# Kernel tuning notes

Hardware: AMD Instinct MI355X
Metric: run time of the kernel (lower is better)

## Reference

```python
import jax, jax.numpy as jnp
import numpy as np

D, H, DFF = 256, 8, 2048
Q, E, WORD = 36, 8, 20
S = 32768 + WORD * E  # 32928 total memory tokens


def _ln(x, g, b, eps=1e-5):
    m = x.mean(-1, keepdims=True)
    v = ((x - m) ** 2).mean(-1, keepdims=True)
    return (x - m) / jnp.sqrt(v + eps) * g + b


def _mha(q, k, v, w_in, b_in, w_out, b_out, nhead, key_pad=None):
    # q: [E,Lq,d], k/v: [E,Lk,d], key_pad: [E,Lk] bool (True = masked)
    e, lq, d = q.shape
    lk = k.shape[1]
    dh = d // nhead
    wq, wk, wv = w_in[:d], w_in[d:2 * d], w_in[2 * d:]
    bq, bk, bv = b_in[:d], b_in[d:2 * d], b_in[2 * d:]
    qp = (q @ wq.T + bq).reshape(e, lq, nhead, dh)
    kp = (k @ wk.T + bk).reshape(e, lk, nhead, dh)
    vp = (v @ wv.T + bv).reshape(e, lk, nhead, dh)
    s = jnp.einsum('eqhd,ekhd->ehqk', qp, kp) / jnp.sqrt(jnp.asarray(dh, qp.dtype))
    if key_pad is not None:
        s = jnp.where(key_pad[:, None, None, :], jnp.asarray(-1e9, s.dtype), s)
    a = jax.nn.softmax(s, axis=-1)
    o = jnp.einsum('ehqk,ekhd->eqhd', a, vp).reshape(e, lq, d)
    return o @ w_out.T + b_out


def setup_inputs() -> dict:
    key = jax.random.key(0)
    ks = jax.random.split(key, 16)
    sc = 0.02
    return {
        'tgt': jax.random.normal(ks[0], (Q, 1, D), jnp.float32),
        'memory': jax.random.normal(ks[1], (S, 1, D), jnp.float32),
        'memory_key_padding_mask': jnp.zeros((1, S), jnp.bool_),
        'pos': jax.random.normal(ks[2], (S, 1, D), jnp.float32),
        'query_pos': jax.random.normal(ks[3], (Q, 1, D), jnp.float32),
        'no_of_exps': E,
        'sa_w_in': sc * jax.random.normal(ks[4], (3 * D, D), jnp.float32),
        'sa_b_in': jnp.zeros((3 * D,), jnp.float32),
        'sa_w_out': sc * jax.random.normal(ks[5], (D, D), jnp.float32),
        'sa_b_out': jnp.zeros((D,), jnp.float32),
        'ca_w_in': sc * jax.random.normal(ks[6], (3 * D, D), jnp.float32),
        'ca_b_in': jnp.zeros((3 * D,), jnp.float32),
        'ca_w_out': sc * jax.random.normal(ks[7], (D, D), jnp.float32),
        'ca_b_out': jnp.zeros((D,), jnp.float32),
        'w1': sc * jax.random.normal(ks[8], (DFF, D), jnp.float32),
        'b1': jnp.zeros((DFF,), jnp.float32),
        'w2': sc * jax.random.normal(ks[9], (D, DFF), jnp.float32),
        'b2': jnp.zeros((D,), jnp.float32),
        'ln1_g': jnp.ones((D,), jnp.float32), 'ln1_b': jnp.zeros((D,), jnp.float32),
        'ln2_g': jnp.ones((D,), jnp.float32), 'ln2_b': jnp.zeros((D,), jnp.float32),
        'ln3_g': jnp.ones((D,), jnp.float32), 'ln3_b': jnp.zeros((D,), jnp.float32),
    }


def reference(tgt, memory, memory_key_padding_mask, pos, query_pos, no_of_exps,
              sa_w_in, sa_b_in, sa_w_out, sa_b_out,
              ca_w_in, ca_b_in, ca_w_out, ca_b_out,
              w1, b1, w2, b2,
              ln1_g, ln1_b, ln2_g, ln2_b, ln3_g, ln3_b):
    e = int(no_of_exps)
    q_len, _, d = tgt.shape
    s_tot = memory.shape[0]
    s_sub = s_tot - WORD * e
    # repeat tgt / query_pos to experts, move expert to batch dim: [E,Q,d]
    x = jnp.broadcast_to(tgt, (q_len, e, d)).transpose(1, 0, 2)
    qp = jnp.broadcast_to(query_pos, (q_len, e, d)).transpose(1, 0, 2)
    # --- self attention (per expert, q=k=tgt+query_pos, v=tgt) ---
    qk = x + qp
    sa = _mha(qk, qk, x, sa_w_in, sa_b_in, sa_w_out, sa_b_out, H)
    x = _ln(x + sa, ln1_g, ln1_b)
    # --- per-expert memory: shared sub_memory + expert word window ---
    mem = memory[:, 0]          # [S,d]
    pmem = pos[:, 0]            # [S,d]
    kpm = memory_key_padding_mask[0]  # [S]
    sub = jnp.broadcast_to(mem[:s_sub], (e, s_sub, d))
    win = mem[s_sub:].reshape(e, WORD, d)
    kv = jnp.concatenate([sub, win], axis=1)            # [E, s_sub+WORD, d]
    psub = jnp.broadcast_to(pmem[:s_sub], (e, s_sub, d))
    pwin = pmem[s_sub:].reshape(e, WORD, d)
    pkv = jnp.concatenate([psub, pwin], axis=1)
    kpm_e = jnp.concatenate([jnp.broadcast_to(kpm[:s_sub], (e, s_sub)),
                             kpm[s_sub:].reshape(e, WORD)], axis=1)
    # --- cross attention ---
    ca = _mha(x + qp, kv + pkv, kv, ca_w_in, ca_b_in, ca_w_out, ca_b_out, H, kpm_e)
    x = _ln(x + ca, ln2_g, ln2_b)
    # --- FFN ---
    ff = jax.nn.relu(x @ w1.T + b1) @ w2.T + b2
    x = _ln(x + ff, ln3_g, ln3_b)
    # torch code cats per-expert [Q,1,d] along dim=1 -> [Q,E,d]
    return x.transpose(1, 0, 2)
```

## Files before the change

### kernel.cpp

```cpp
#include <hip/hip_runtime.h>
#include <math.h>

#define D_ 256
#define H_ 8
#define Q_ 36
#define E_ 8
#define WORD_ 20
#define S_ 32928
#define SSUB_ 32768
#define DFF_ 2048
#define NCHUNK 256
#define KC 128

typedef unsigned int u32;
typedef unsigned short u16;
typedef unsigned long long u64;
typedef float f4 __attribute__((ext_vector_type(4)));
typedef short bf8 __attribute__((ext_vector_type(8)));
typedef short s4v __attribute__((ext_vector_type(4)));

__device__ __forceinline__ u16 f2bf(float f) {
    u32 u = __float_as_uint(f);
    u32 r = u + 0x7fffu + ((u >> 16) & 1u);
    return (u16)(r >> 16);
}
__device__ __forceinline__ float bf2f(u16 h) { return __uint_as_float(((u32)h) << 16); }

__device__ __forceinline__ f4 mfma16(bf8 a, bf8 b, f4 c) {
    return __builtin_amdgcn_mfma_f32_16x16x32_bf16(a, b, c, 0, 0, 0);
}

__device__ __forceinline__ void block_ln_stats(float v, float* red, float* red2, int tid,
                                               float& mean, float& var) {
    red[tid] = v; red2[tid] = v * v;
    __syncthreads();
    for (int st = 128; st > 0; st >>= 1) {
        if (tid < st) { red[tid] += red[tid + st]; red2[tid] += red2[tid + st]; }
        __syncthreads();
    }
    mean = red[0] * (1.f / 256.f);
    var = red2[0] * (1.f / 256.f) - mean * mean;
    __syncthreads();
}

__global__ void __launch_bounds__(256) k_wcvt(const float* __restrict__ caw,
                                              const float* __restrict__ w1,
                                              const float* __restrict__ w2,
                                              u16* __restrict__ wkvbf,
                                              u16* __restrict__ w1bf,
                                              u16* __restrict__ w2bf) {
    int i = (blockIdx.x * 256 + threadIdx.x) * 4;
    const float* src; u16* dst; int off;
    if (i < 131072) { src = caw + 65536; dst = wkvbf; off = i; }
    else if (i < 655360) { src = w1; dst = w1bf; off = i - 131072; }
    else { src = w2; dst = w2bf; off = i - 655360; }
    float4 v = *(const float4*)(src + off);
    ushort4 o;
    o.x = f2bf(v.x); o.y = f2bf(v.y); o.z = f2bf(v.z); o.w = f2bf(v.w);
    *(ushort4*)(dst + off) = o;
}

__global__ void __launch_bounds__(512, 2) k_kv(const float* __restrict__ mem,
                                               const float* __restrict__ pos,
                                               const u16* __restrict__ wkvbf,
                                               const float* __restrict__ cab,
                                               u16* __restrict__ Kca, u16* __restrict__ Vca) {
    __shared__ u16 smem[4][64 * 64];
    char* const base = (char*)smem;
    const int tid = threadIdx.x;
    const int lane = tid & 63, wid = tid >> 6;
    const int lr = lane & 15, lg = lane >> 4;
    const int s0 = blockIdx.x * 64;
    const int kv = wid >> 2;
    const int cb = (wid & 3) * 64;
    const u16* wb = wkvbf + kv * 65536;

    const int srow = tid >> 3;
    const int scol = (tid & 7) * 8;
    int sg = s0 + srow; if (sg >= S_) sg = S_ - 1;
    const float* mp = mem + (u64)sg * 256 + scol;
    const float* pp = pos + (u64)sg * 256 + scol;
    const int sboff = (srow * 128 + scol * 2) ^ ((srow & 7) << 4);

    f4 acc[4][4];
#pragma unroll
    for (int i = 0; i < 4; i++)
#pragma unroll
        for (int j = 0; j < 4; j++) acc[i][j] = (f4){0.f, 0.f, 0.f, 0.f};

    float4 Lm0[2], Lm1[2], Lp0[2], Lp1[2];
    Lm0[0] = *(const float4*)(mp);
    Lm1[0] = *(const float4*)(mp + 4);
    Lp0[0] = *(const float4*)(pp);
    Lp1[0] = *(const float4*)(pp + 4);

#pragma unroll
    for (int ks = 0; ks < 4; ks++) {
        const int cur = ks & 1, nxt = cur ^ 1;
        if (ks < 3) {
            Lm0[nxt] = *(const float4*)(mp + (ks + 1) * 64);
            Lm1[nxt] = *(const float4*)(mp + (ks + 1) * 64 + 4);
            Lp0[nxt] = *(const float4*)(pp + (ks + 1) * 64);
            Lp1[nxt] = *(const float4*)(pp + (ks + 1) * 64 + 4);
        }
        u16 tk[8], tv[8];
        tk[0] = f2bf(Lm0[cur].x + Lp0[cur].x); tk[1] = f2bf(Lm0[cur].y + Lp0[cur].y);
        tk[2] = f2bf(Lm0[cur].z + Lp0[cur].z); tk[3] = f2bf(Lm0[cur].w + Lp0[cur].w);
        tk[4] = f2bf(Lm1[cur].x + Lp1[cur].x); tk[5] = f2bf(Lm1[cur].y + Lp1[cur].y);
        tk[6] = f2bf(Lm1[cur].z + Lp1[cur].z); tk[7] = f2bf(Lm1[cur].w + Lp1[cur].w);
        tv[0] = f2bf(Lm0[cur].x); tv[1] = f2bf(Lm0[cur].y);
        tv[2] = f2bf(Lm0[cur].z); tv[3] = f2bf(Lm0[cur].w);
        tv[4] = f2bf(Lm1[cur].x); tv[5] = f2bf(Lm1[cur].y);
        tv[6] = f2bf(Lm1[cur].z); tv[7] = f2bf(Lm1[cur].w);
        char* AbK = base + cur * 16384;
        char* AbV = AbK + 8192;
        *(bf8*)(AbK + sboff) = *(bf8*)tk;
        *(bf8*)(AbV + sboff) = *(bf8*)tv;
        __syncthreads();
        char* Ab = kv ? AbV : AbK;
#pragma unroll
        for (int kk = 0; kk < 2; kk++) {
            bf8 af[4], bfr[4];
#pragma unroll
            for (int b = 0; b < 4; b++) {
                int row = b * 16 + lr;
                af[b] = *(const bf8*)(Ab + ((row * 128 + kk * 64 + lg * 16) ^ ((row & 7) << 4)));
            }
#pragma unroll
            for (int a = 0; a < 4; a++) {
                int n = cb + a * 16 + lr;
                bfr[a] = *(const bf8*)(wb + (u64)n * 256 + ks * 64 + kk * 32 + lg * 8);
            }
            if (kv == 0) {
#pragma unroll
                for (int a = 0; a < 4; a++)
#pragma unroll
                    for (int b = 0; b < 4; b++)
                        acc[a][b] = mfma16(bfr[a], af[b], acc[a][b]);
            } else {
#pragma unroll
                for (int a = 0; a < 4; a++)
#pragma unroll
                    for (int b = 0; b < 4; b++)
                        acc[a][b] = mfma16(af[a], bfr[b], acc[a][b]);
            }
        }
        __syncthreads();
    }

    if (kv == 0) {
        float biasK[4][4];
#pragma unroll
        for (int a = 0; a < 4; a++)
#pragma unroll
            for (int r = 0; r < 4; r++) biasK[a][r] = cab[256 + cb + a * 16 + lg * 4 + r];
#pragma unroll
        for (int a = 0; a < 4; a++)
#pragma unroll
            for (int b = 0; b < 4; b++) {
                int nn = cb + a * 16 + lg * 4;
                int s = b * 16 + lr;
                u16 t4[4];
#pragma unroll
                for (int r = 0; r < 4; r++) t4[r] = f2bf(acc[a][b][r] + biasK[a][r]);
                *(s4v*)(base + ((s * 512 + nn * 2) ^ ((s & 7) << 4))) = *(s4v*)t4;
            }
    }
    __syncthreads();
#pragma unroll
    for (int i = 0; i < 4; i++) {
        int c = tid + i * 512;
        int s = c >> 5, oct = c & 31;
        if (s0 + s < S_) {
            bf8 v = *(const bf8*)(base + ((s * 512 + oct * 16) ^ ((s & 7) << 4)));
            int h = oct >> 2, nl = (oct & 3) * 8;
            *(bf8*)(Kca + ((u64)h * S_ + s0 + s) * 32 + nl) = v;
        }
    }
    __syncthreads();
    if (kv == 1) {
#pragma unroll
        for (int b = 0; b < 4; b++) {
            int n = cb + b * 16 + lr;
            float bias = cab[512 + n];
#pragma unroll
            for (int a = 0; a < 4; a++) {
                int sb = a * 16 + lg * 4;
                u16 t4[4];
#pragma unroll
                for (int r = 0; r < 4; r++) t4[r] = f2bf(acc[a][b][r] + bias);
                *(s4v*)(base + ((n * 128 + sb * 2) ^ ((n & 7) << 4))) = *(s4v*)t4;
            }
        }
    }
    __syncthreads();
#pragma unroll
    for (int i = 0; i < 4; i++) {
        int c = tid + i * 512;
        int n = c >> 3, oct = c & 7;
        int ss = s0 + oct * 8;
        if (ss < S_) {
            bf8 v = *(const bf8*)(base + ((n * 128 + oct * 16) ^ ((n & 7) << 4)));
            *(bf8*)(Vca + (u64)n * S_ + ss) = v;
        }
    }
}

__global__ void __launch_bounds__(256) k_saproj(const float* __restrict__ tgt,
                                                const float* __restrict__ qpos,
                                                const float* __restrict__ w,
                                                const float* __restrict__ bvec,
                                                float* __restrict__ qkv) {
    int bx = blockIdx.x;
    int mat = bx / 36, row = bx % 36;
    int n = threadIdx.x;
    __shared__ float xr[256];
    float tv = tgt[row * 256 + n];
    xr[n] = (mat < 2) ? tv + qpos[row * 256 + n] : tv;
    __syncthreads();
    const float* wr_ = w + (u64)(mat * 256 + n) * 256;
    float acc = bvec[mat * 256 + n];
    for (int k = 0; k < 256; k++) acc += xr[k] * wr_[k];
    qkv[(u64)bx * 256 + n] = acc;
}

__global__ void __launch_bounds__(256) k_saattn(const float* __restrict__ qkv,
                                                float* __restrict__ osa) {
    int hh = blockIdx.x;
    int tid = threadIdx.x;
    __shared__ float qh[36][32], kh[36][32], vh[36][32];
    __shared__ float sc[36][40];
    for (int i = tid; i < 36 * 32; i += 256) {
        int rr = i >> 5, dd = i & 31;
        qh[rr][dd] = qkv[(u64)(0 + rr) * 256 + hh * 32 + dd];
        kh[rr][dd] = qkv[(u64)(36 + rr) * 256 + hh * 32 + dd];
        vh[rr][dd] = qkv[(u64)(72 + rr) * 256 + hh * 32 + dd];
    }
    __syncthreads();
    for (int i = tid; i < 36 * 36; i += 256) {
        int qi = i / 36, ki = i % 36;
        float s = 0.f;
        for (int k2 = 0; k2 < 32; k2++) s += qh[qi][k2] * kh[ki][k2];
        sc[qi][ki] = s * 0.17677669529663687f;
    }
    __syncthreads();
    if (tid < 36) {
        float mx = sc[tid][0];
        for (int k = 1; k < 36; k++) mx = fmaxf(mx, sc[tid][k]);
        float zz = 0.f;
        for (int k = 0; k < 36; k++) { float p = __expf(sc[tid][k] - mx); sc[tid][k] = p; zz += p; }
        float inv = 1.f / zz;
        for (int k = 0; k < 36; k++) sc[tid][k] *= inv;
    }
    __syncthreads();
    for (int i = tid; i < 36 * 32; i += 256) {
        int qi = i >> 5, dd = i & 31;
        float s = 0.f;
        for (int k2 = 0; k2 < 36; k2++) s += sc[qi][k2] * vh[k2][dd];
        osa[(u64)qi * 256 + hh * 32 + dd] = s;
    }
}

__global__ void __launch_bounds__(256) k_ln1(const float* __restrict__ osa,
                                             const float* __restrict__ tgt,
                                             const float* __restrict__ qpos,
                                             const float* __restrict__ swout,
                                             const float* __restrict__ sbout,
                                             const float* __restrict__ g1,
                                             const float* __restrict__ b1ln,
                                             const float* __restrict__ caw,
                                             const float* __restrict__ cab,
                                             float* __restrict__ x1, float* __restrict__ qca) {
    int q = blockIdx.x;
    int n = threadIdx.x;
    __shared__ float orow[256], xq[256], red[256], red2[256];
    orow[n] = osa[(u64)q * 256 + n];
    __syncthreads();
    float acc = sbout[n] + tgt[q * 256 + n];
    const float* wr_ = swout + (u64)n * 256;
    for (int k = 0; k < 256; k++) acc += orow[k] * wr_[k];
    float mean, var;
    block_ln_stats(acc, red, red2, n, mean, var);
    float rstd = rsqrtf(var + 1e-5f);
    float val = (acc - mean) * rstd * g1[n] + b1ln[n];
    x1[(u64)q * 256 + n] = val;
    xq[n] = val + qpos[q * 256 + n];
    __syncthreads();
    float a2 = cab[n];
    const float* wr2 = caw + (u64)n * 256;
    for (int k = 0; k < 256; k++) a2 += xq[k] * wr2[k];
    qca[(u64)q * 256 + n] = a2 * 0.17677669529663687f;
}

__global__ void __launch_bounds__(256) k_flash(const float* __restrict__ qca,
                                               const u16* __restrict__ Kca,
                                               const u16* __restrict__ Vca,
                                               u16* __restrict__ nump,
                                               float* __restrict__ mzp) {
    __shared__ u16 pT[4][48 * 64];
    const int tid = threadIdx.x;
    const int lane = tid & 63, wslot = tid >> 6;
    const int gw = blockIdx.x * 4 + wslot;
    const int h = gw >> 8, chunk = gw & 255;
    const int lr = lane & 15, lg = lane >> 4;
    char* pb = (char*)pT[wslot];

    bf8 qf[3];
#pragma unroll
    for (int nt = 0; nt < 3; nt++) {
        int q = nt * 16 + lr;
        u16 t8[8];
        if (q < Q_) {
            const float* p = qca + (u64)q * 256 + h * 32 + lg * 8;
#pragma unroll
            for (int j = 0; j < 8; j++) t8[j] = f2bf(p[j]);
        } else {
#pragma unroll
            for (int j = 0; j < 8; j++) t8[j] = 0;
        }
        qf[nt] = *(bf8*)t8;
    }
    f4 numT[2][3];
#pragma unroll
    for (int mi = 0; mi < 2; mi++)
#pragma unroll
        for (int nt = 0; nt < 3; nt++) numT[mi][nt] = (f4){0.f, 0.f, 0.f, 0.f};
    float mrun[3] = {-3e38f, -3e38f, -3e38f};
    float zl[3] = {0.f, 0.f, 0.f};
    const int base = chunk * KC;
    const f4 z4 = (f4){0.f, 0.f, 0.f, 0.f};

    for (int b = 0; b < 2; b++) {
        int kb0 = base + b * 64;
        f4 st[4][3];
#pragma unroll
        for (int kt = 0; kt < 4; kt++) {
            bf8 af = *(const bf8*)(Kca + ((u64)h * S_ + kb0 + kt * 16 + lr) * 32 + lg * 8);
#pragma unroll
            for (int nt = 0; nt < 3; nt++) st[kt][nt] = mfma16(af, qf[nt], z4);
        }
#pragma unroll
        for (int nt = 0; nt < 3; nt++) {
            float mx = -3e38f;
#pragma unroll
            for (int kt = 0; kt < 4; kt++)
#pragma unroll
                for (int r = 0; r < 4; r++) mx = fmaxf(mx, st[kt][nt][r]);
            mx = fmaxf(mx, __shfl_xor(mx, 16));
            mx = fmaxf(mx, __shfl_xor(mx, 32));
            float mnew = fmaxf(mrun[nt], mx);
            float al = __expf(mrun[nt] - mnew);
            mrun[nt] = mnew;
            float zs = 0.f;
#pragma unroll
            for (int kt = 0; kt < 4; kt++)
#pragma unroll
                for (int r = 0; r < 4; r++) {
                    float p = __expf(st[kt][nt][r] - mnew);
                    st[kt][nt][r] = p;
                    zs += p;
                }
            zl[nt] = zl[nt] * al + zs;
#pragma unroll
            for (int mi = 0; mi < 2; mi++)
#pragma unroll
                for (int r = 0; r < 4; r++) numT[mi][nt][r] *= al;
            int qrow = nt * 16 + lr;
            int swz = (qrow & 7) << 4;
#pragma unroll
            for (int kt = 0; kt < 4; kt++)
#pragma unroll
                for (int r = 0; r < 4; r += 2) {
                    int keyl = kt * 16 + lg * 4 + r;
                    u32 pk = (u32)f2bf(st[kt][nt][r]) | ((u32)f2bf(st[kt][nt][r + 1]) << 16);
                    *(u32*)(pb + qrow * 128 + ((keyl * 2) ^ swz)) = pk;
                }
        }
#pragma unroll
        for (int kb = 0; kb < 2; kb++) {
            bf8 pf[3];
#pragma unroll
            for (int nt = 0; nt < 3; nt++) {
                int qrow = nt * 16 + lr;
                pf[nt] = *(const bf8*)(pb + qrow * 128 + ((kb * 64 + lg * 16) ^ ((qrow & 7) << 4)));
            }
#pragma unroll
            for (int mi = 0; mi < 2; mi++) {
                bf8 vf = *(const bf8*)(Vca + ((u64)(h * 32 + mi * 16 + lr)) * S_ + kb0 + kb * 32 + lg * 8);
#pragma unroll
                for (int nt = 0; nt < 3; nt++) numT[mi][nt] = mfma16(vf, pf[nt], numT[mi][nt]);
            }
        }
    }
#pragma unroll
    for (int nt = 0; nt < 3; nt++) {
        float z = zl[nt];
        z += __shfl_xor(z, 16);
        z += __shfl_xor(z, 32);
        int q = nt * 16 + lr;
        if (lg == 0 && q < Q_) {
            u64 o = ((u64)(h * 36 + q) * NCHUNK + chunk) * 2;
            mzp[o] = mrun[nt];
            mzp[o + 1] = z;
        }
    }
#pragma unroll
    for (int mi = 0; mi < 2; mi++)
#pragma unroll
        for (int nt = 0; nt < 3; nt++) {
            int q = nt * 16 + lr;
            if (q < Q_) {
#pragma unroll
                for (int r = 0; r < 4; r++)
                    nump[((u64)(h * 36 + q) * NCHUNK + chunk) * 32 + mi * 16 + lg * 4 + r] =
                        f2bf(numT[mi][nt][r]);
            }
        }
}

__global__ void __launch_bounds__(64) k_merge(const float* __restrict__ mzp,
                                              const u16* __restrict__ nump,
                                              float* __restrict__ ssum) {
    int idx = blockIdx.x;
    int lane = threadIdx.x;
    float m[4], z[4];
#pragma unroll
    for (int j = 0; j < 4; j++) {
        m[j] = mzp[((u64)idx * NCHUNK + j * 64 + lane) * 2];
        z[j] = mzp[((u64)idx * NCHUNK + j * 64 + lane) * 2 + 1];
    }
    float M = fmaxf(fmaxf(m[0], m[1]), fmaxf(m[2], m[3]));
    for (int o = 1; o < 64; o <<= 1) M = fmaxf(M, __shfl_xor(M, o));
    float w[4], Z = 0.f;
#pragma unroll
    for (int j = 0; j < 4; j++) { w[j] = __expf(m[j] - M); Z += z[j] * w[j]; }
    for (int o = 1; o < 64; o <<= 1) Z += __shfl_xor(Z, o);
    __shared__ float buf[64][33];
#pragma unroll
    for (int d = 0; d < 32; d++) {
        float s = 0.f;
#pragma unroll
        for (int j = 0; j < 4; j++)
            s += bf2f(nump[((u64)idx * NCHUNK + j * 64 + lane) * 32 + d]) * w[j];
        buf[lane][d] = s;
    }
    __syncthreads();
    if (lane < 32) {
        float s = 0.f;
        for (int c = 0; c < 64; c++) s += buf[c][lane];
        ssum[(u64)idx * 34 + 2 + lane] = s;
    }
    if (lane == 0) { ssum[(u64)idx * 34] = M; ssum[(u64)idx * 34 + 1] = Z; }
}

__global__ void __launch_bounds__(256) k_combine(const float* __restrict__ qca,
                                                 const u16* __restrict__ Kca,
                                                 const u16* __restrict__ Vca,
                                                 const float* __restrict__ ssum,
                                                 const float* __restrict__ x1,
                                                 const float* __restrict__ wout,
                                                 const float* __restrict__ bout,
                                                 const float* __restrict__ g2,
                                                 const float* __restrict__ b2ln,
                                                 float* __restrict__ x2f, u16* __restrict__ x2h) {
    int bx = blockIdx.x;
    int e = bx / 36, q = bx % 36;
    int tid = threadIdx.x;
    __shared__ float pw[8][20], Mh[8], Zh[8], Ssc[8], o[256], red[256], red2[256];
    int h = tid >> 5, d = tid & 31;
    if (d < WORD_) {
        int key = SSUB_ + e * WORD_ + d;
        const float* qp = qca + (u64)q * 256 + h * 32;
        const u16* kp = Kca + ((u64)h * S_ + key) * 32;
        float s = 0.f;
        for (int k = 0; k < 32; k++) s += qp[k] * bf2f(kp[k]);
        pw[h][d] = s;
    }
    __syncthreads();
    if (tid < 8) {
        int hh = tid, ih = hh * 36 + q;
        float Ms = ssum[(u64)ih * 34], Zs = ssum[(u64)ih * 34 + 1];
        float mw = pw[hh][0];
        for (int w = 1; w < WORD_; w++) mw = fmaxf(mw, pw[hh][w]);
        float Me = fmaxf(Ms, mw);
        float Zw = 0.f;
        for (int w = 0; w < WORD_; w++) { float p = __expf(pw[hh][w] - Me); pw[hh][w] = p; Zw += p; }
        float sc = __expf(Ms - Me);
        Mh[hh] = Me; Zh[hh] = Zs * sc + Zw; Ssc[hh] = sc;
    }
    __syncthreads();
    {
        int ih = h * 36 + q;
        float num = ssum[(u64)ih * 34 + 2 + d] * Ssc[h];
        const u16* vp = Vca + ((u64)(h * 32 + d)) * S_ + SSUB_ + e * WORD_;
        for (int w = 0; w < WORD_; w++) num += pw[h][w] * bf2f(vp[w]);
        o[tid] = num / Zh[h];
    }
    __syncthreads();
    int n = tid;
    float acc = bout[n] + x1[(u64)q * 256 + n];
    const float* wr_ = wout + (u64)n * 256;
    for (int k = 0; k < 256; k++) acc += o[k] * wr_[k];
    float mean, var;
    block_ln_stats(acc, red, red2, n, mean, var);
    float rstd = rsqrtf(var + 1e-5f);
    float val = (acc - mean) * rstd * g2[n] + b2ln[n];
    x2f[(u64)bx * 256 + n] = val;
    x2h[(u64)bx * 256 + n] = f2bf(val);
}

__global__ void __launch_bounds__(64) k_ffn1(const u16* __restrict__ x2h,
                                             const u16* __restrict__ w1bf,
                                             const float* __restrict__ b1,
                                             u16* __restrict__ hbuf) {
    const int lane = threadIdx.x & 63;
    const int lr = lane & 15, lg = lane >> 4;
    const int s0 = blockIdx.x * 16, n0 = blockIdx.y * 64;

    f4 acc[4];
#pragma unroll
    for (int ni = 0; ni < 4; ni++) acc[ni] = (f4){0.f, 0.f, 0.f, 0.f};

#pragma unroll
    for (int k0 = 0; k0 < 8; k0++) {
        bf8 a = *(const bf8*)(x2h + (u64)(s0 + lr) * 256 + k0 * 32 + lg * 8);
#pragma unroll
        for (int ni = 0; ni < 4; ni++) {
            bf8 b = *(const bf8*)(w1bf + (u64)(n0 + ni * 16 + lr) * 256 + k0 * 32 + lg * 8);
            acc[ni] = mfma16(b, a, acc[ni]);
        }
    }
#pragma unroll
    for (int ni = 0; ni < 4; ni++) {
        int n = n0 + ni * 16 + lg * 4;
        float4 bi = *(const float4*)(b1 + n);
        u16 t4[4];
        t4[0] = f2bf(fmaxf(acc[ni][0] + bi.x, 0.f));
        t4[1] = f2bf(fmaxf(acc[ni][1] + bi.y, 0.f));
        t4[2] = f2bf(fmaxf(acc[ni][2] + bi.z, 0.f));
        t4[3] = f2bf(fmaxf(acc[ni][3] + bi.w, 0.f));
        *(s4v*)(hbuf + (u64)(s0 + lr) * 2048 + n) = *(s4v*)t4;
    }
}

__global__ void __launch_bounds__(256) k_ffn2(const u16* __restrict__ hbuf,
                                              const u16* __restrict__ w2bf,
                                              float* __restrict__ ypart) {
    const int tid = threadIdx.x;
    const int lane = tid & 63, wid = tid >> 6;
    const int lr = lane & 15, lg = lane >> 4;
    const int s0 = blockIdx.x * 16, kc = blockIdx.y;

    f4 acc[4];
#pragma unroll
    for (int ni = 0; ni < 4; ni++) acc[ni] = (f4){0.f, 0.f, 0.f, 0.f};

#pragma unroll
    for (int k0 = 0; k0 < 8; k0++) {
        bf8 a = *(const bf8*)(hbuf + (u64)(s0 + lr) * 2048 + kc * 256 + k0 * 32 + lg * 8);
#pragma unroll
        for (int ni = 0; ni < 4; ni++) {
            bf8 b = *(const bf8*)(w2bf + (u64)(wid * 64 + ni * 16 + lr) * 2048 + kc * 256 + k0 * 32 + lg * 8);
            acc[ni] = mfma16(b, a, acc[ni]);
        }
    }
#pragma unroll
    for (int ni = 0; ni < 4; ni++) {
        int n = wid * 64 + ni * 16 + lg * 4;
        *(f4*)(ypart + ((u64)kc * 288 + s0 + lr) * 256 + n) = acc[ni];
    }
}

__global__ void __launch_bounds__(256) k_ln3(const float* __restrict__ ypart,
                                             const float* __restrict__ b2,
                                             const float* __restrict__ x2f,
                                             const float* __restrict__ g3,
                                             const float* __restrict__ b3,
                                             float* __restrict__ out) {
    int r = blockIdx.x;
    int e = r / 36, q = r - e * 36;
    int n = threadIdx.x;
    __shared__ float red[256], red2[256];
    float v = x2f[(u64)r * 256 + n] + b2[n];
#pragma unroll
    for (int kc = 0; kc < 8; kc++) v += ypart[((u64)kc * 288 + r) * 256 + n];
    float mean, var;
    block_ln_stats(v, red, red2, n, mean, var);
    float rstd = rsqrtf(var + 1e-5f);
    float val = (v - mean) * rstd * g3[n] + b3[n];
    out[((u64)q * E_ + e) * 256 + n] = val;
}

extern "C" void kernel_launch(void* const* d_in, const int* in_sizes, int n_in,
                              void* d_out, int out_size, void* d_ws, size_t ws_size,
                              hipStream_t stream) {
    const float* tgt = (const float*)d_in[0];
    const float* mem = (const float*)d_in[1];
    const float* pos = (const float*)d_in[3];
    const float* qpos = (const float*)d_in[4];
    const float* sa_w_in = (const float*)d_in[6];
    const float* sa_b_in = (const float*)d_in[7];
    const float* sa_w_out = (const float*)d_in[8];
    const float* sa_b_out = (const float*)d_in[9];
    const float* ca_w_in = (const float*)d_in[10];
    const float* ca_b_in = (const float*)d_in[11];
    const float* ca_w_out = (const float*)d_in[12];
    const float* ca_b_out = (const float*)d_in[13];
    const float* w1 = (const float*)d_in[14];
    const float* b1 = (const float*)d_in[15];
    const float* w2 = (const float*)d_in[16];
    const float* b2 = (const float*)d_in[17];
    const float* g1 = (const float*)d_in[18];
    const float* bb1 = (const float*)d_in[19];
    const float* g2 = (const float*)d_in[20];
    const float* bb2 = (const float*)d_in[21];
    const float* g3 = (const float*)d_in[22];
    const float* bb3 = (const float*)d_in[23];
    float* out = (float*)d_out;

    char* ws = (char*)d_ws;
    u16* Kca    = (u16*)(ws);
    u16* Vca    = (u16*)(ws + 16859136);
    u16* wkvbf  = (u16*)(ws + 33718272);
    u16* w1bf   = (u16*)(ws + 33980416);
    u16* w2bf   = (u16*)(ws + 35028992);
    float* qkv  = (float*)(ws + 36077568);
    float* osa  = (float*)(ws + 36188160);
    float* x1   = (float*)(ws + 36225024);
    float* qca  = (float*)(ws + 36261888);
    u16* nump   = (u16*)(ws + 36298752);
    u16* hbuf   = (u16*)(ws + 36298752);
    float* ypart= (float*)(ws + 37478400);
    float* mzp  = (float*)(ws + 41017344);
    float* ssum = (float*)(ws + 41607168);
    float* x2f  = (float*)(ws + 41646336);
    u16* x2h    = (u16*)(ws + 41941248);

    hipLaunchKernelGGL(k_wcvt, dim3(1152), dim3(256), 0, stream, ca_w_in, w1, w2, wkvbf, w1bf, w2bf);
    hipLaunchKernelGGL(k_kv, dim3(515), dim3(512), 0, stream, mem, pos, wkvbf, ca_b_in, Kca, Vca);
    hipLaunchKernelGGL(k_saproj, dim3(108), dim3(256), 0, stream, tgt, qpos, sa_w_in, sa_b_in, qkv);
    hipLaunchKernelGGL(k_saattn, dim3(8), dim3(256), 0, stream, qkv, osa);
    hipLaunchKernelGGL(k_ln1, dim3(36), dim3(256), 0, stream, osa, tgt, qpos, sa_w_out, sa_b_out,
                       g1, bb1, ca_w_in, ca_b_in, x1, qca);
    hipLaunchKernelGGL(k_flash, dim3(512), dim3(256), 0, stream, qca, Kca, Vca, nump, mzp);
    hipLaunchKernelGGL(k_merge, dim3(288), dim3(64), 0, stream, mzp, nump, ssum);
    hipLaunchKernelGGL(k_combine, dim3(288), dim3(256), 0, stream, qca, Kca, Vca, ssum, x1,
                       ca_w_out, ca_b_out, g2, bb2, x2f, x2h);
    hipLaunchKernelGGL(k_ffn1, dim3(18, 32), dim3(64), 0, stream, x2h, w1bf, b1, hbuf);
    hipLaunchKernelGGL(k_ffn2, dim3(18, 8), dim3(256), 0, stream, hbuf, w2bf, ypart);
    hipLaunchKernelGGL(k_ln3, dim3(288), dim3(256), 0, stream, ypart, b2, x2f, g3, bb3, out);
}
```

Baseline: 139.8 us.

## Preload full K tile in k_kv and use transposed bf16 small-GEMV weights

```diff
diff --git a/kernel.cpp b/kernel.cpp
--- a/kernel.cpp
+++ b/kernel.cpp
@@ -44,29 +44,59 @@
 }
 
 __global__ void __launch_bounds__(256) k_wcvt(const float* __restrict__ caw,
+                                              const float* __restrict__ saw,
+                                              const float* __restrict__ sow,
+                                              const float* __restrict__ cow,
                                               const float* __restrict__ w1,
                                               const float* __restrict__ w2,
                                               u16* __restrict__ wkvbf,
                                               u16* __restrict__ w1bf,
-                                              u16* __restrict__ w2bf) {
-    int i = (blockIdx.x * 256 + threadIdx.x) * 4;
-    const float* src; u16* dst; int off;
-    if (i < 131072) { src = caw + 65536; dst = wkvbf; off = i; }
-    else if (i < 655360) { src = w1; dst = w1bf; off = i - 131072; }
-    else { src = w2; dst = w2bf; off = i - 655360; }
-    float4 v = *(const float4*)(src + off);
-    ushort4 o;
-    o.x = f2bf(v.x); o.y = f2bf(v.y); o.z = f2bf(v.z); o.w = f2bf(v.w);
-    *(ushort4*)(dst + off) = o;
-}
-
-__global__ void __launch_bounds__(512, 2) k_kv(const float* __restrict__ mem,
+                                              u16* __restrict__ w2bf,
+                                              u16* __restrict__ saT,
+                                              u16* __restrict__ soT,
+                                              u16* __restrict__ caqT,
+                                              u16* __restrict__ coT) {
+    long i = ((long)blockIdx.x * 256 + threadIdx.x) * 4;
+    if (i < 1179648) {
+        const float* src; u16* dst; long off;
+        if (i < 131072) { src = caw + 65536; dst = wkvbf; off = i; }
+        else if (i < 655360) { src = w1; dst = w1bf; off = i - 131072; }
+        else { src = w2; dst = w2bf; off = i - 655360; }
+        float4 v = *(const float4*)(src + off);
+        ushort4 o;
+        o.x = f2bf(v.x); o.y = f2bf(v.y); o.z = f2bf(v.z); o.w = f2bf(v.w);
+        *(ushort4*)(dst + off) = o;
+    } else {
+        long j = i - 1179648;
+#pragma unroll
+        for (int t = 0; t < 4; t++) {
+            long e = j + t;
+            if (e < 196608) {
+                int n = e >> 8, k = e & 255;
+                saT[k * 768 + n] = f2bf(saw[e]);
+            } else if (e < 262144) {
+                long e2 = e - 196608; int n = e2 >> 8, k = e2 & 255;
+                soT[k * 256 + n] = f2bf(sow[e2]);
+            } else if (e < 327680) {
+                long e2 = e - 262144; int n = e2 >> 8, k = e2 & 255;
+                caqT[k * 256 + n] = f2bf(caw[e2]);
+            } else if (e < 393216) {
+                long e2 = e - 327680; int n = e2 >> 8, k = e2 & 255;
+                coT[k * 256 + n] = f2bf(cow[e2]);
+            }
+        }
+    }
+}
+
+__global__ void __launch_bounds__(512, 4) k_kv(const float* __restrict__ mem,
                                                const float* __restrict__ pos,
                                                const u16* __restrict__ wkvbf,
                                                const float* __restrict__ cab,
                                                u16* __restrict__ Kca, u16* __restrict__ Vca) {
-    __shared__ u16 smem[4][64 * 64];
-    char* const base = (char*)smem;
+    __shared__ u16 AK[64 * 256];
+    __shared__ u16 AV[64 * 256];
+    char* const bK = (char*)AK;
+    char* const bV = (char*)AV;
     const int tid = threadIdx.x;
     const int lane = tid & 63, wid = tid >> 6;
     const int lr = lane & 15, lg = lane >> 4;
@@ -76,11 +106,35 @@
     const u16* wb = wkvbf + kv * 65536;
 
     const int srow = tid >> 3;
-    const int scol = (tid & 7) * 8;
+    const int scol8 = (tid & 7) * 8;
     int sg = s0 + srow; if (sg >= S_) sg = S_ - 1;
-    const float* mp = mem + (u64)sg * 256 + scol;
-    const float* pp = pos + (u64)sg * 256 + scol;
-    const int sboff = (srow * 128 + scol * 2) ^ ((srow & 7) << 4);
+    const float* mp = mem + (u64)sg * 256 + scol8;
+    const float* pp = pos + (u64)sg * 256 + scol8;
+
+    float4 M0[4], M1[4], P0[4], P1[4];
+#pragma unroll
+    for (int g = 0; g < 4; g++) {
+        M0[g] = *(const float4*)(mp + g * 64);
+        M1[g] = *(const float4*)(mp + g * 64 + 4);
+        P0[g] = *(const float4*)(pp + g * 64);
+        P1[g] = *(const float4*)(pp + g * 64 + 4);
+    }
+#pragma unroll
+    for (int g = 0; g < 4; g++) {
+        u16 tk[8], tv[8];
+        tk[0] = f2bf(M0[g].x + P0[g].x); tk[1] = f2bf(M0[g].y + P0[g].y);
+        tk[2] = f2bf(M0[g].z + P0[g].z); tk[3] = f2bf(M0[g].w + P0[g].w);
+        tk[4] = f2bf(M1[g].x + P1[g].x); tk[5] = f2bf(M1[g].y + P1[g].y);
+        tk[6] = f2bf(M1[g].z + P1[g].z); tk[7] = f2bf(M1[g].w + P1[g].w);
+        tv[0] = f2bf(M0[g].x); tv[1] = f2bf(M0[g].y);
+        tv[2] = f2bf(M0[g].z); tv[3] = f2bf(M0[g].w);
+        tv[4] = f2bf(M1[g].x); tv[5] = f2bf(M1[g].y);
+        tv[6] = f2bf(M1[g].z); tv[7] = f2bf(M1[g].w);
+        int boff = (srow * 512 + (scol8 + g * 64) * 2) ^ ((srow & 7) << 4);
+        *(bf8*)(bK + boff) = *(bf8*)tk;
+        *(bf8*)(bV + boff) = *(bf8*)tv;
+    }
+    __syncthreads();
 
     f4 acc[4][4];
 #pragma unroll
@@ -88,65 +142,35 @@
 #pragma unroll
         for (int j = 0; j < 4; j++) acc[i][j] = (f4){0.f, 0.f, 0.f, 0.f};
 
-    float4 Lm0[2], Lm1[2], Lp0[2], Lp1[2];
-    Lm0[0] = *(const float4*)(mp);
-    Lm1[0] = *(const float4*)(mp + 4);
-    Lp0[0] = *(const float4*)(pp);
-    Lp1[0] = *(const float4*)(pp + 4);
-
-#pragma unroll
-    for (int ks = 0; ks < 4; ks++) {
-        const int cur = ks & 1, nxt = cur ^ 1;
-        if (ks < 3) {
-            Lm0[nxt] = *(const float4*)(mp + (ks + 1) * 64);
-            Lm1[nxt] = *(const float4*)(mp + (ks + 1) * 64 + 4);
-            Lp0[nxt] = *(const float4*)(pp + (ks + 1) * 64);
-            Lp1[nxt] = *(const float4*)(pp + (ks + 1) * 64 + 4);
-        }
-        u16 tk[8], tv[8];
-        tk[0] = f2bf(Lm0[cur].x + Lp0[cur].x); tk[1] = f2bf(Lm0[cur].y + Lp0[cur].y);
-        tk[2] = f2bf(Lm0[cur].z + Lp0[cur].z); tk[3] = f2bf(Lm0[cur].w + Lp0[cur].w);
-        tk[4] = f2bf(Lm1[cur].x + Lp1[cur].x); tk[5] = f2bf(Lm1[cur].y + Lp1[cur].y);
-        tk[6] = f2bf(Lm1[cur].z + Lp1[cur].z); tk[7] = f2bf(Lm1[cur].w + Lp1[cur].w);
-        tv[0] = f2bf(Lm0[cur].x); tv[1] = f2bf(Lm0[cur].y);
-        tv[2] = f2bf(Lm0[cur].z); tv[3] = f2bf(Lm0[cur].w);
-        tv[4] = f2bf(Lm1[cur].x); tv[5] = f2bf(Lm1[cur].y);
-        tv[6] = f2bf(Lm1[cur].z); tv[7] = f2bf(Lm1[cur].w);
-        char* AbK = base + cur * 16384;
-        char* AbV = AbK + 8192;
-        *(bf8*)(AbK + sboff) = *(bf8*)tk;
-        *(bf8*)(AbV + sboff) = *(bf8*)tv;
-        __syncthreads();
-        char* Ab = kv ? AbV : AbK;
-#pragma unroll
-        for (int kk = 0; kk < 2; kk++) {
-            bf8 af[4], bfr[4];
-#pragma unroll
-            for (int b = 0; b < 4; b++) {
-                int row = b * 16 + lr;
-                af[b] = *(const bf8*)(Ab + ((row * 128 + kk * 64 + lg * 16) ^ ((row & 7) << 4)));
-            }
-#pragma unroll
-            for (int a = 0; a < 4; a++) {
-                int n = cb + a * 16 + lr;
-                bfr[a] = *(const bf8*)(wb + (u64)n * 256 + ks * 64 + kk * 32 + lg * 8);
-            }
-            if (kv == 0) {
-#pragma unroll
-                for (int a = 0; a < 4; a++)
-#pragma unroll
-                    for (int b = 0; b < 4; b++)
-                        acc[a][b] = mfma16(bfr[a], af[b], acc[a][b]);
-            } else {
-#pragma unroll
-                for (int a = 0; a < 4; a++)
-#pragma unroll
-                    for (int b = 0; b < 4; b++)
-                        acc[a][b] = mfma16(af[a], bfr[b], acc[a][b]);
-            }
-        }
-        __syncthreads();
-    }
+    char* Ab = kv ? bV : bK;
+#pragma unroll
+    for (int kk = 0; kk < 8; kk++) {
+        bf8 af[4], bfr[4];
+#pragma unroll
+        for (int b = 0; b < 4; b++) {
+            int row = b * 16 + lr;
+            af[b] = *(const bf8*)(Ab + ((row * 512 + kk * 64 + lg * 16) ^ ((row & 7) << 4)));
+        }
+#pragma unroll
+        for (int a = 0; a < 4; a++) {
+            int n = cb + a * 16 + lr;
+            bfr[a] = *(const bf8*)(wb + (u64)n * 256 + kk * 32 + lg * 8);
+        }
+        if (kv == 0) {
+#pragma unroll
+            for (int a = 0; a < 4; a++)
+#pragma unroll
+                for (int b = 0; b < 4; b++)
+                    acc[a][b] = mfma16(bfr[a], af[b], acc[a][b]);
+        } else {
+#pragma unroll
+            for (int a = 0; a < 4; a++)
+#pragma unroll
+                for (int b = 0; b < 4; b++)
+                    acc[a][b] = mfma16(af[a], bfr[b], acc[a][b]);
+        }
+    }
+    __syncthreads();
 
     if (kv == 0) {
         float biasK[4][4];
@@ -163,8 +187,22 @@
                 u16 t4[4];
 #pragma unroll
                 for (int r = 0; r < 4; r++) t4[r] = f2bf(acc[a][b][r] + biasK[a][r]);
-                *(s4v*)(base + ((s * 512 + nn * 2) ^ ((s & 7) << 4))) = *(s4v*)t4;
+                *(s4v*)(bK + ((s * 512 + nn * 2) ^ ((s & 7) << 4))) = *(s4v*)t4;
             }
+    } else {
+#pragma unroll
+        for (int b = 0; b < 4; b++) {
+            int n = cb + b * 16 + lr;
+            float bias = cab[512 + n];
+#pragma unroll
+            for (int a = 0; a < 4; a++) {
+                int sb = a * 16 + lg * 4;
+                u16 t4[4];
+#pragma unroll
+                for (int r = 0; r < 4; r++) t4[r] = f2bf(acc[a][b][r] + bias);
+                *(s4v*)(bV + ((n * 128 + sb * 2) ^ ((n & 7) << 4))) = *(s4v*)t4;
+            }
+        }
     }
     __syncthreads();
 #pragma unroll
@@ -172,35 +210,18 @@
         int c = tid + i * 512;
         int s = c >> 5, oct = c & 31;
         if (s0 + s < S_) {
-            bf8 v = *(const bf8*)(base + ((s * 512 + oct * 16) ^ ((s & 7) << 4)));
+            bf8 v = *(const bf8*)(bK + ((s * 512 + oct * 16) ^ ((s & 7) << 4)));
             int h = oct >> 2, nl = (oct & 3) * 8;
             *(bf8*)(Kca + ((u64)h * S_ + s0 + s) * 32 + nl) = v;
         }
     }
-    __syncthreads();
-    if (kv == 1) {
-#pragma unroll
-        for (int b = 0; b < 4; b++) {
-            int n = cb + b * 16 + lr;
-            float bias = cab[512 + n];
-#pragma unroll
-            for (int a = 0; a < 4; a++) {
-                int sb = a * 16 + lg * 4;
-                u16 t4[4];
-#pragma unroll
-                for (int r = 0; r < 4; r++) t4[r] = f2bf(acc[a][b][r] + bias);
-                *(s4v*)(base + ((n * 128 + sb * 2) ^ ((n & 7) << 4))) = *(s4v*)t4;
-            }
-        }
-    }
-    __syncthreads();
 #pragma unroll
     for (int i = 0; i < 4; i++) {
         int c = tid + i * 512;
         int n = c >> 3, oct = c & 7;
         int ss = s0 + oct * 8;
         if (ss < S_) {
-            bf8 v = *(const bf8*)(base + ((n * 128 + oct * 16) ^ ((n & 7) << 4)));
+            bf8 v = *(const bf8*)(bV + ((n * 128 + oct * 16) ^ ((n & 7) << 4)));
             *(bf8*)(Vca + (u64)n * S_ + ss) = v;
         }
     }
@@ -208,7 +229,7 @@
 
 __global__ void __launch_bounds__(256) k_saproj(const float* __restrict__ tgt,
                                                 const float* __restrict__ qpos,
-                                                const float* __restrict__ w,
+                                                const u16* __restrict__ saT,
                                                 const float* __restrict__ bvec,
                                                 float* __restrict__ qkv) {
     int bx = blockIdx.x;
@@ -218,9 +239,9 @@
     float tv = tgt[row * 256 + n];
     xr[n] = (mat < 2) ? tv + qpos[row * 256 + n] : tv;
     __syncthreads();
-    const float* wr_ = w + (u64)(mat * 256 + n) * 256;
+    const u16* wt = saT + mat * 256 + n;
     float acc = bvec[mat * 256 + n];
-    for (int k = 0; k < 256; k++) acc += xr[k] * wr_[k];
+    for (int k = 0; k < 256; k++) acc += xr[k] * bf2f(wt[(u64)k * 768]);
     qkv[(u64)bx * 256 + n] = acc;
 }
 
@@ -264,11 +285,11 @@
 __global__ void __launch_bounds__(256) k_ln1(const float* __restrict__ osa,
                                              const float* __restrict__ tgt,
                                              const float* __restrict__ qpos,
-                                             const float* __restrict__ swout,
+                                             const u16* __restrict__ soT,
                                              const float* __restrict__ sbout,
                                              const float* __restrict__ g1,
                                              const float* __restrict__ b1ln,
-                                             const float* __restrict__ caw,
+                                             const u16* __restrict__ caqT,
                                              const float* __restrict__ cab,
                                              float* __restrict__ x1, float* __restrict__ qca) {
     int q = blockIdx.x;
@@ -277,8 +298,7 @@
     orow[n] = osa[(u64)q * 256 + n];
     __syncthreads();
     float acc = sbout[n] + tgt[q * 256 + n];
-    const float* wr_ = swout + (u64)n * 256;
-    for (int k = 0; k < 256; k++) acc += orow[k] * wr_[k];
+    for (int k = 0; k < 256; k++) acc += orow[k] * bf2f(soT[(u64)k * 256 + n]);
     float mean, var;
     block_ln_stats(acc, red, red2, n, mean, var);
     float rstd = rsqrtf(var + 1e-5f);
@@ -287,8 +307,7 @@
     xq[n] = val + qpos[q * 256 + n];
     __syncthreads();
     float a2 = cab[n];
-    const float* wr2 = caw + (u64)n * 256;
-    for (int k = 0; k < 256; k++) a2 += xq[k] * wr2[k];
+    for (int k = 0; k < 256; k++) a2 += xq[k] * bf2f(caqT[(u64)k * 256 + n]);
     qca[(u64)q * 256 + n] = a2 * 0.17677669529663687f;
 }
 
@@ -458,7 +477,7 @@
                                                  const u16* __restrict__ Vca,
                                                  const float* __restrict__ ssum,
                                                  const float* __restrict__ x1,
-                                                 const float* __restrict__ wout,
+                                                 const u16* __restrict__ coT,
                                                  const float* __restrict__ bout,
                                                  const float* __restrict__ g2,
                                                  const float* __restrict__ b2ln,
@@ -499,8 +518,7 @@
     __syncthreads();
     int n = tid;
     float acc = bout[n] + x1[(u64)q * 256 + n];
-    const float* wr_ = wout + (u64)n * 256;
-    for (int k = 0; k < 256; k++) acc += o[k] * wr_[k];
+    for (int k = 0; k < 256; k++) acc += o[k] * bf2f(coT[(u64)k * 256 + n]);
     float mean, var;
     block_ln_stats(acc, red, red2, n, mean, var);
     float rstd = rsqrtf(var + 1e-5f);
@@ -629,23 +647,28 @@
     float* x1   = (float*)(ws + 36225024);
     float* qca  = (float*)(ws + 36261888);
     u16* nump   = (u16*)(ws + 36298752);
+    u16* saT    = (u16*)(ws + 36298752);
+    u16* soT    = (u16*)(ws + 36691968);
+    u16* caqT   = (u16*)(ws + 36823040);
     u16* hbuf   = (u16*)(ws + 36298752);
     float* ypart= (float*)(ws + 37478400);
     float* mzp  = (float*)(ws + 41017344);
     float* ssum = (float*)(ws + 41607168);
     float* x2f  = (float*)(ws + 41646336);
     u16* x2h    = (u16*)(ws + 41941248);
-
-    hipLaunchKernelGGL(k_wcvt, dim3(1152), dim3(256), 0, stream, ca_w_in, w1, w2, wkvbf, w1bf, w2bf);
+    u16* coT    = (u16*)(ws + 42088704);
+
+    hipLaunchKernelGGL(k_wcvt, dim3(1536), dim3(256), 0, stream, ca_w_in, sa_w_in, sa_w_out,
+                       ca_w_out, w1, w2, wkvbf, w1bf, w2bf, saT, soT, caqT, coT);
     hipLaunchKernelGGL(k_kv, dim3(515), dim3(512), 0, stream, mem, pos, wkvbf, ca_b_in, Kca, Vca);
-    hipLaunchKernelGGL(k_saproj, dim3(108), dim3(256), 0, stream, tgt, qpos, sa_w_in, sa_b_in, qkv);
+    hipLaunchKernelGGL(k_saproj, dim3(108), dim3(256), 0, stream, tgt, qpos, saT, sa_b_in, qkv);
     hipLaunchKernelGGL(k_saattn, dim3(8), dim3(256), 0, stream, qkv, osa);
-    hipLaunchKernelGGL(k_ln1, dim3(36), dim3(256), 0, stream, osa, tgt, qpos, sa_w_out, sa_b_out,
-                       g1, bb1, ca_w_in, ca_b_in, x1, qca);
+    hipLaunchKernelGGL(k_ln1, dim3(36), dim3(256), 0, stream, osa, tgt, qpos, soT, sa_b_out,
+                       g1, bb1, caqT, ca_b_in, x1, qca);
     hipLaunchKernelGGL(k_flash, dim3(512), dim3(256), 0, stream, qca, Kca, Vca, nump, mzp);
     hipLaunchKernelGGL(k_merge, dim3(288), dim3(64), 0, stream, mzp, nump, ssum);
     hipLaunchKernelGGL(k_combine, dim3(288), dim3(256), 0, stream, qca, Kca, Vca, ssum, x1,
-                       ca_w_out, ca_b_out, g2, bb2, x2f, x2h);
+                       coT, ca_b_out, g2, bb2, x2f, x2h);
     hipLaunchKernelGGL(k_ffn1, dim3(18, 32), dim3(64), 0, stream, x2h, w1bf, b1, hbuf);
     hipLaunchKernelGGL(k_ffn2, dim3(18, 8), dim3(256), 0, stream, hbuf, w2bf, ypart);
     hipLaunchKernelGGL(k_ln3, dim3(288), dim3(256), 0, stream, ypart, b2, x2f, g3, bb3, out);
```

Result: slower. 195.9 us (+40.1%).
